# Performance work log

Measured on AMD Instinct MI355X. Metric: run time of the kernel, lower is better.

Reference implementation:

```python
import jax, jax.numpy as jnp
import numpy as np

DIM = 256   # model dim (forced by gate Linear(32,4): d = 32 = DIM//H)
H = 8       # heads (hard-coded by mask.repeat(1,8,1,1))
D = DIM // H
B = 256     # batch
NS = 100    # skeleton tokens (sub-block size)
NQ = 64     # query tokens
N = NS + NQ # 164
NE = 4      # experts
HID = 50    # expert hidden
LN_EPS = 1e-5


def setup_inputs() -> dict:
    key = jax.random.key(0)
    ks = jax.random.split(key, 12)
    s = 0.02
    return {
        "x": jax.random.normal(ks[0], (B, N, DIM), jnp.float32),
        "mask": jax.random.randint(ks[1], (B, N), 0, 2).astype(bool),
        "w_qk_s": jax.random.normal(ks[2], (DIM, 2 * DIM), jnp.float32) * s,
        "w_qk_q": jax.random.normal(ks[3], (DIM, 2 * DIM), jnp.float32) * s,
        "w_v": jax.random.normal(ks[4], (DIM, DIM), jnp.float32) * s,
        "w_gate": jax.random.normal(ks[5], (D, NE), jnp.float32) * s,
        "b_gate": jnp.zeros((NE,), jnp.float32),
        "ln_gamma": jnp.ones((NE,), jnp.float32),
        "ln_beta": jnp.zeros((NE,), jnp.float32),
        "w1": jax.random.normal(ks[6], (NE, NS, HID), jnp.float32) * s,
        "b1": jnp.zeros((NE, HID), jnp.float32),
        "w2": jax.random.normal(ks[7], (NE, HID, NS), jnp.float32) * s,
        "b2": jnp.zeros((NE, NS), jnp.float32),
        "w_out": jax.random.normal(ks[8], (DIM, DIM), jnp.float32) * s,
        "b_out": jnp.zeros((DIM,), jnp.float32),
    }


def reference(x, mask, w_qk_s, w_qk_q, w_v, w_gate, b_gate, ln_gamma, ln_beta,
              w1, b1, w2, b2, w_out, b_out):
    b, n, dim = x.shape
    scale = dim ** -0.5  # scale_with_head=False -> dim**-0.5

    def to_heads(t):  # (b, m, H*D) -> (b, H, m, D)
        return t.reshape(b, -1, H, D).transpose(0, 2, 1, 3)

    # separate qk projections for skeleton (first 100) vs query (last 64) tokens
    q_s, k_s = jnp.split(x[:, :NS] @ w_qk_s, 2, axis=-1)
    q_q, k_q = jnp.split(x[:, NS:] @ w_qk_q, 2, axis=-1)
    q = jnp.concatenate([to_heads(q_s), to_heads(q_q)], axis=2)  # (b,H,N,D)
    k = jnp.concatenate([to_heads(k_s), to_heads(k_q)], axis=2)
    v = to_heads(x @ w_v)

    # gates: RAW reshape of x (b,n,H*D) -> (b,H,n,D) (memory reinterpretation,
    # as in torch x.reshape), detached, sliced to first 100 'rows'
    gx = jax.lax.stop_gradient(x).reshape(b, H, n, D)[:, :, :NS, :]
    g = gx @ w_gate + b_gate                              # (b,H,100,4)
    mu = g.mean(-1, keepdims=True)
    var = g.var(-1, keepdims=True)
    g = (g - mu) / jnp.sqrt(var + LN_EPS) * ln_gamma + ln_beta
    gates = jax.nn.softmax(g, axis=-1)                    # (b,H,100,4)

    dots = jnp.einsum('bhid,bhjd->bhij', q, k) * scale    # (b,H,N,N)
    mask_value = -jnp.finfo(dots.dtype).max
    dots = jnp.where(mask[:, None, None, :], mask_value, dots)

    # soft-MoE over the 100x100 sub-block (experts applied along key axis)
    attn_q = dots[:, :, :NS, :NS]                         # (b,H,100,100)
    h1 = jax.nn.relu(jnp.einsum('bhij,ejk->bheik', jax.nn.relu(attn_q), w1)
                     + b1[:, None, :])                    # (b,H,4,100,50)
    eo = jax.nn.relu(jnp.einsum('bheik,ekj->bheij', h1, w2)
                     + b2[:, None, :])                    # (b,H,4,100,100)
    moes = jnp.einsum('bheij,bhie->bhij', eo, gates)      # (b,H,100,100)

    dots = dots.at[:, :, :NS, :NS].add(moes)
    attn = jax.nn.softmax(dots, axis=-1)
    out = jnp.einsum('bhij,bhjd->bhid', attn, v)          # (b,H,N,D)
    out = out.transpose(0, 2, 1, 3).reshape(b, n, dim)
    return out @ w_out + b_out
```

## Files before the change

### kernel.cpp

```cpp
#include <hip/hip_runtime.h>

typedef __bf16 bf16x8 __attribute__((ext_vector_type(8)));
typedef __bf16 bf16x4 __attribute__((ext_vector_type(4)));
typedef float  f32x4  __attribute__((ext_vector_type(4)));

__device__ __forceinline__ bf16x8 ldb8(const __bf16* p) {
    return *reinterpret_cast<const bf16x8*>(p);
}
__device__ __forceinline__ bf16x8 zero8() {
    bf16x8 z;
    #pragma unroll
    for (int i = 0; i < 8; i++) z[i] = (__bf16)0.f;
    return z;
}
__device__ __forceinline__ __bf16 ldw(const void* p, int i, int m) {
    return m ? (__bf16)((const float*)p)[i] : ((const __bf16*)p)[i];
}
__device__ __forceinline__ bf16x8 ldx8(const void* p, size_t ei, int m) {
    if (m) {
        const float* f = (const float*)p + ei;
        f32x4 a = *reinterpret_cast<const f32x4*>(f);
        f32x4 b = *reinterpret_cast<const f32x4*>(f + 4);
        bf16x8 r;
        #pragma unroll
        for (int u = 0; u < 4; u++) { r[u] = (__bf16)a[u]; r[4 + u] = (__bf16)b[u]; }
        return r;
    }
    return ldb8((const __bf16*)p + ei);
}

__global__ __launch_bounds__(256) void detect_kernel(
    const void* x, const void* mask, int* modes, unsigned* maskb)
{
    __shared__ int v32bad, v16bad, sbad;
    __shared__ unsigned mb[24];
    const int t = threadIdx.x, bid = blockIdx.x;
    if (t == 0) { v32bad = 0; v16bad = 0; sbad = 0; }
    if (t < 24) mb[t] = ((t % 6) == 5) ? 0xFFFFFFF0u : 0u;
    __syncthreads();
    const unsigned int* mw = (const unsigned int*)mask;
    int b32 = 0, b16 = 0;
    for (int i = t; i < 10496; i += 256) {
        unsigned int w = mw[i];
        if (!(w == 0u || w == 1u || w == 0x3F800000u)) b32++;
        unsigned int h0 = w & 0xFFFFu, h1 = w >> 16;
        if (!(h0 == 0u || h0 == 1u || h0 == 0x3F80u)) b16++;
        if (!(h1 == 0u || h1 == 1u || h1 == 0x3F80u)) b16++;
    }
    if (b32) atomicAdd(&v32bad, b32);
    if (b16) atomicAdd(&v16bad, b16);
    if (bid == 0) {
        const unsigned int* xw = (const unsigned int*)x;
        int bad = 0;
        for (int i = t; i < 2048; i += 256) {
            unsigned int w = xw[i];
            unsigned int el = (w >> 7) & 0xFF, eh = (w >> 23) & 0xFF;
            if (el >= 0x94 || el == 0xFF) bad++;
            if (eh >= 0x94 || eh == 0xFF) bad++;
        }
        if (bad) atomicAdd(&sbad, bad);
    }
    __syncthreads();
    const int mmode = (v32bad == 0) ? 0 : ((v16bad == 0) ? 2 : 1);
    if (bid == 0 && t == 0) { modes[0] = (sbad > 64) ? 1 : 0; modes[1] = mmode; }
    const int lo = bid * 656;
    for (int i2 = t; i2 < 656; i2 += 256) {
        int i = lo + i2;
        int val;
        if (mmode == 0)      val = (((const int*)mask)[i] != 0);
        else if (mmode == 2) val = (((const unsigned short*)mask)[i] != 0);
        else                 val = (((const unsigned char*)mask)[i] != 0);
        if (val) {
            int ib = i2 / 164, jb = i2 - ib * 164;
            atomicOr(&mb[ib * 6 + (jb >> 5)], 1u << (jb & 31));
        }
    }
    __syncthreads();
    if (t < 24) maskb[bid * 24 + t] = mb[t];
}

__global__ __launch_bounds__(256) void prep_kernel(
    const void* wqks, const void* wqkq, const void* wv, const void* w1,
    const void* w2, const void* wout, const void* wg, const void* bg,
    const void* lng, const void* lnb, const void* b1, const void* b2,
    const void* bout, const int* __restrict__ modes,
    __bf16* __restrict__ Wts, __bf16* __restrict__ Wtq,
    __bf16* __restrict__ w1t, __bf16* __restrict__ w2t,
    __bf16* __restrict__ wot, __bf16* __restrict__ wsm)
{
    const int m = modes[0];
    int i = blockIdx.x * 256 + threadIdx.x;
    if (i < 196608) {
        int n = i >> 8, k = i & 255;
        __bf16 vs, vq;
        if (n < 512) { vs = ldw(wqks, k * 512 + n, m); vq = ldw(wqkq, k * 512 + n, m); }
        else         { vs = ldw(wv, k * 256 + (n - 512), m); vq = vs; }
        Wts[i] = vs; Wtq[i] = vq;
        return;
    }
    i -= 196608;
    if (i < 32768) {
        int e = i >> 13, r = i & 8191, n = r >> 7, k = r & 127;
        __bf16 v = (__bf16)0.f;
        if (n < 50) {
            if (k < 100)       v = ldw(w1, (e * 100 + k) * 50 + n, m);
            else if (k == 100) v = ldw(b1, e * 50 + n, m);
        }
        w1t[i] = v;
        return;
    }
    i -= 32768;
    if (i < 28672) {
        int e = i / 7168, r = i % 7168, n = r >> 6, k = r & 63;
        __bf16 v = (__bf16)0.f;
        if (n < 100) {
            if (k < 50)       v = ldw(w2, (e * 50 + k) * 100 + n, m);
            else if (k == 50) v = ldw(b2, e * 100 + n, m);
        }
        w2t[i] = v;
        return;
    }
    i -= 28672;
    if (i < 65536) {
        int n = i >> 8, k = i & 255;
        wot[i] = ldw(wout, k * 256 + n, m);
        return;
    }
    i -= 65536;
    if (i < 996) {
        __bf16 v;
        if (i < 128)      v = ldw(wg, i, m);
        else if (i < 132) v = ldw(bg, i - 128, m);
        else if (i < 136) v = ldw(lng, i - 132, m);
        else if (i < 140) v = ldw(lnb, i - 136, m);
        else if (i < 340) v = ldw(b1, i - 140, m);
        else if (i < 740) v = ldw(b2, i - 340, m);
        else              v = ldw(bout, i - 740, m);
        wsm[i] = v;
    }
}

__global__ __launch_bounds__(256, 2) void qkv_kernel(
    const void* __restrict__ x, const __bf16* __restrict__ Wts,
    const __bf16* __restrict__ Wtq, const __bf16* __restrict__ wsm,
    const int* __restrict__ modes,
    __bf16* __restrict__ q, __bf16* __restrict__ k, __bf16* __restrict__ vt,
    float* __restrict__ gates)
{
    __shared__ __bf16 xs[32][264];
    __shared__ float wgf[128];
    __shared__ float gcst[12];
    const int m = modes[0];
    const int b = blockIdx.y;
    const int mt = blockIdx.x >> 1;
    const int half = blockIdx.x & 1;
    const __bf16* Wt = (mt < 4) ? Wts : Wtq;
    const int rbase = (mt < 4) ? mt * 32 : 100 + (mt - 4) * 32;
    const int tid = threadIdx.x;

    if (tid < 128) wgf[tid] = (float)wsm[tid];
    if (tid < 12)  gcst[tid] = (float)wsm[128 + tid];
    for (int c = tid; c < 1024; c += 256) {
        int row = c >> 5, part = c & 31;
        bf16x8 val = ldx8(x, ((size_t)b * 164 + rbase + row) * 256 + part * 8, m);
        *reinterpret_cast<bf16x8*>(&xs[row][part * 8]) = val;
    }
    __syncthreads();

    if (half == 0) {
        int jg = rbase * 8 + tid;
        int h = jg / 164;
        int j = jg - h * 164;
        if (j < 100) {
            const __bf16* xp = &xs[tid >> 3][(tid & 7) * 32];
            float g[4] = {gcst[0], gcst[1], gcst[2], gcst[3]};
            #pragma unroll
            for (int p = 0; p < 4; p++) {
                bf16x8 xv = ldb8(xp + p * 8);
                #pragma unroll
                for (int u = 0; u < 8; u++) {
                    float f = (float)xv[u];
                    #pragma unroll
                    for (int e = 0; e < 4; e++) g[e] += f * wgf[(p * 8 + u) * 4 + e];
                }
            }
            float mu = 0.25f * (g[0] + g[1] + g[2] + g[3]);
            float var = 0.25f * ((g[0]-mu)*(g[0]-mu) + (g[1]-mu)*(g[1]-mu) +
                                 (g[2]-mu)*(g[2]-mu) + (g[3]-mu)*(g[3]-mu));
            float is = rsqrtf(var + 1e-5f);
            float mx = -3.0e38f;
            #pragma unroll
            for (int e = 0; e < 4; e++) {
                g[e] = (g[e] - mu) * is * gcst[4 + e] + gcst[8 + e];
                mx = fmaxf(mx, g[e]);
            }
            float s = 0.f;
            #pragma unroll
            for (int e = 0; e < 4; e++) { g[e] = __expf(g[e] - mx); s += g[e]; }
            float inv = 1.f / s;
            float4 gv = make_float4(g[0]*inv, g[1]*inv, g[2]*inv, g[3]*inv);
            *reinterpret_cast<float4*>(&gates[((size_t)(b * 8 + h) * 100 + j) * 4]) = gv;
        }
    }

    const int w = tid >> 6, l = tid & 63, lr = l & 15, lc = l >> 4;
    f32x4 acc[2][6];
    #pragma unroll
    for (int ms = 0; ms < 2; ms++)
        #pragma unroll
        for (int nt = 0; nt < 6; nt++) acc[ms][nt] = (f32x4){0.f, 0.f, 0.f, 0.f};

    #pragma unroll
    for (int kt = 0; kt < 8; kt++) {
        bf16x8 a0 = ldb8(&xs[lr][kt * 32 + lc * 8]);
        bf16x8 a1 = ldb8(&xs[16 + lr][kt * 32 + lc * 8]);
        #pragma unroll
        for (int nt = 0; nt < 6; nt++) {
            bf16x8 bb = ldb8(Wt + (size_t)(half * 384 + w * 96 + nt * 16 + lr) * 256 + kt * 32 + lc * 8);
            acc[0][nt] = __builtin_amdgcn_mfma_f32_16x16x32_bf16(a0, bb, acc[0][nt], 0, 0, 0);
            acc[1][nt] = __builtin_amdgcn_mfma_f32_16x16x32_bf16(a1, bb, acc[1][nt], 0, 0, 0);
        }
    }
    #pragma unroll
    for (int ms = 0; ms < 2; ms++) {
        #pragma unroll
        for (int nt = 0; nt < 6; nt++) {
            int c = half * 384 + w * 96 + nt * 16 + lr;
            int i0 = rbase + ms * 16 + lc * 4;
            if (c < 512) {
                __bf16* dst; int ch;
                if (c < 256) { dst = q; ch = c; }
                else         { dst = k; ch = c - 256; }
                int hh = ch >> 5, d = ch & 31;
                #pragma unroll
                for (int r = 0; r < 4; r++) {
                    int i = i0 + r;
                    if (mt >= 4 || i < 100)
                        dst[(((size_t)b * 8 + hh) * 164 + i) * 32 + d] = (__bf16)acc[ms][nt][r];
                }
            } else {
                int ch = c - 512, hh = ch >> 5, d = ch & 31;
                if (mt >= 4 || i0 < 100) {
                    bf16x4 pv;
                    #pragma unroll
                    for (int r = 0; r < 4; r++) pv[r] = (__bf16)acc[ms][nt][r];
                    *reinterpret_cast<bf16x4*>(&vt[((size_t)(b * 8 + hh) * 32 + d) * 176 + i0]) = pv;
                }
            }
        }
    }
}

__global__ __launch_bounds__(256, 4) void attn_kernel(
    const __bf16* __restrict__ qg, const __bf16* __restrict__ kg,
    const __bf16* __restrict__ vtg, const float* __restrict__ gatesg,
    const unsigned* __restrict__ maskbg, const __bf16* __restrict__ w1t,
    const __bf16* __restrict__ w2t, __bf16* __restrict__ ohg)
{
    __shared__ __align__(16) __bf16 lds[20352];
    const int RS_OFF = 7040;
    const int P_OFF  = 7040;
    const int H1_OFF = 15744;

    const int bh = blockIdx.x, rt = blockIdx.y, b = bh >> 3, tid = threadIdx.x;
    const int w = tid >> 6, l = tid & 63, lr = l & 15, lc = l >> 4;
    const int m0 = w * 16;

    const __bf16* kbase = kg + (size_t)bh * 164 * 32;
    for (int c = tid; c < 704; c += 256) {
        int row = c >> 2, part = c & 3;
        bf16x8 val = (row < 164) ? ldb8(kbase + row * 32 + part * 8) : zero8();
        *reinterpret_cast<bf16x8*>(&lds[row * 40 + part * 8]) = val;
    }
    const unsigned* mbp = maskbg + b * 6;
    unsigned mbits = 0;
    #pragma unroll
    for (int nt = 0; nt < 11; nt++)
        mbits |= ((mbp[nt >> 1] >> (((nt & 1) << 4) + lr)) & 1u) << nt;
    int qrow = rt * 64 + m0 + lr; if (qrow > 163) qrow = 163;
    bf16x8 afq = ldb8(qg + ((size_t)bh * 164 + qrow) * 32 + lc * 8);
    __syncthreads();

    f32x4 raw[11];
    __builtin_amdgcn_s_setprio(1);
    #pragma unroll
    for (int nt = 0; nt < 11; nt++) {
        bf16x8 bf = ldb8(&lds[(nt * 16 + lr) * 40 + lc * 8]);
        f32x4 acc = {0.f, 0.f, 0.f, 0.f};
        acc = __builtin_amdgcn_mfma_f32_16x16x32_bf16(afq, bf, acc, 0, 0, 0);
        bool bad = (mbits >> nt) & 1;
        #pragma unroll
        for (int r = 0; r < 4; r++)
            raw[nt][r] = bad ? -1e30f : acc[r] * 0.0625f;
    }
    __builtin_amdgcn_s_setprio(0);

    if (rt < 2) {
        #pragma unroll
        for (int nt = 0; nt < 8; nt++) {
            int j = nt * 16 + lr;
            #pragma unroll
            for (int r = 0; r < 4; r++) {
                float v = raw[nt][r];
                v = (v < 0.f) ? 0.f : v;
                if (j >= 100) v = (j == 100) ? 1.f : 0.f;
                lds[RS_OFF + (m0 + lc * 4 + r) * 136 + j] = (__bf16)v;
            }
        }
    }
    __syncthreads();

    const __bf16* vtb = vtg + (size_t)bh * 32 * 176;
    #pragma unroll
    for (int p = 0; p < 3; p++) {
        int c = tid + p * 256;
        int row = c / 24, jc = c - row * 24, j0 = jc * 8;
        bf16x8 vv;
        if (j0 < 164) {
            vv = ldb8(vtb + row * 176 + j0);
            if (j0 == 160) { vv[4] = (__bf16)0.f; vv[5] = (__bf16)0.f; vv[6] = (__bf16)0.f; vv[7] = (__bf16)0.f; }
        } else vv = zero8();
        *reinterpret_cast<bf16x8*>(&lds[row * 200 + j0]) = vv;
    }

    if (rt < 2) {
        const int gi0 = rt * 64 + m0 + lc * 4;
        for (int e = 0; e < 4; e++) {
            bf16x8 sa[4];
            #pragma unroll
            for (int kt = 0; kt < 4; kt++)
                sa[kt] = ldb8(&lds[RS_OFF + (m0 + lr) * 136 + kt * 32 + lc * 8]);
            #pragma unroll
            for (int nt = 0; nt < 4; nt++) {
                f32x4 acc = {0.f, 0.f, 0.f, 0.f};
                __builtin_amdgcn_s_setprio(1);
                #pragma unroll
                for (int kt = 0; kt < 4; kt++) {
                    bf16x8 bb = ldb8(w1t + (size_t)(e * 64 + nt * 16 + lr) * 128 + kt * 32 + lc * 8);
                    acc = __builtin_amdgcn_mfma_f32_16x16x32_bf16(sa[kt], bb, acc, 0, 0, 0);
                }
                __builtin_amdgcn_s_setprio(0);
                int n = nt * 16 + lr;
                #pragma unroll
                for (int r = 0; r < 4; r++) {
                    float v = acc[r];
                    if (v < 0.f) v = 0.f;
                    if (n == 50) v = 1.f;
                    lds[H1_OFF + (m0 + lc * 4 + r) * 72 + n] = (__bf16)v;
                }
            }
            bf16x8 ha0 = ldb8(&lds[H1_OFF + (m0 + lr) * 72 + lc * 8]);
            bf16x8 ha1 = ldb8(&lds[H1_OFF + (m0 + lr) * 72 + 32 + lc * 8]);
            float gt[4];
            #pragma unroll
            for (int r = 0; r < 4; r++) {
                int gi = gi0 + r;
                gt[r] = (gi < 100) ? gatesg[((size_t)bh * 100 + gi) * 4 + e] : 0.f;
            }
            #pragma unroll
            for (int nt = 0; nt < 7; nt++) {
                f32x4 acc = {0.f, 0.f, 0.f, 0.f};
                __builtin_amdgcn_s_setprio(1);
                bf16x8 bb0 = ldb8(w2t + (size_t)(e * 112 + nt * 16 + lr) * 64 + lc * 8);
                acc = __builtin_amdgcn_mfma_f32_16x16x32_bf16(ha0, bb0, acc, 0, 0, 0);
                bf16x8 bb1 = ldb8(w2t + (size_t)(e * 112 + nt * 16 + lr) * 64 + 32 + lc * 8);
                acc = __builtin_amdgcn_mfma_f32_16x16x32_bf16(ha1, bb1, acc, 0, 0, 0);
                __builtin_amdgcn_s_setprio(0);
                #pragma unroll
                for (int r = 0; r < 4; r++) {
                    float v = acc[r];
                    if (v < 0.f) v = 0.f;
                    raw[nt][r] += v * gt[r];
                }
            }
        }
    }
    __syncthreads();

    #pragma unroll
    for (int r = 0; r < 4; r++) {
        float m2 = raw[0][r];
        #pragma unroll
        for (int nt = 1; nt < 11; nt++) m2 = fmaxf(m2, raw[nt][r]);
        m2 = fmaxf(m2, __shfl_xor(m2, 1, 64));
        m2 = fmaxf(m2, __shfl_xor(m2, 2, 64));
        m2 = fmaxf(m2, __shfl_xor(m2, 4, 64));
        m2 = fmaxf(m2, __shfl_xor(m2, 8, 64));
        float s2 = 0.f;
        #pragma unroll
        for (int nt = 0; nt < 11; nt++) {
            float ev = __expf(raw[nt][r] - m2);
            raw[nt][r] = ev;
            s2 += ev;
        }
        s2 += __shfl_xor(s2, 1, 64);
        s2 += __shfl_xor(s2, 2, 64);
        s2 += __shfl_xor(s2, 4, 64);
        s2 += __shfl_xor(s2, 8, 64);
        float inv = (s2 > 0.f) ? 1.f / s2 : 0.f;
        #pragma unroll
        for (int nt = 0; nt < 11; nt++)
            lds[P_OFF + (m0 + lc * 4 + r) * 200 + nt * 16 + lr] = (__bf16)(raw[nt][r] * inv);
        lds[P_OFF + (m0 + lc * 4 + r) * 200 + 176 + lr] = (__bf16)0.f;
    }
    __syncthreads();

    int gi = rt * 64 + m0 + lr;
    #pragma unroll
    for (int nt = 0; nt < 2; nt++) {
        f32x4 acc = {0.f, 0.f, 0.f, 0.f};
        __builtin_amdgcn_s_setprio(1);
        #pragma unroll
        for (int kt = 0; kt < 6; kt++) {
            bf16x8 va = ldb8(&lds[(nt * 16 + lr) * 200 + kt * 32 + lc * 8]);
            bf16x8 pb = ldb8(&lds[P_OFF + (m0 + lr) * 200 + kt * 32 + lc * 8]);
            acc = __builtin_amdgcn_mfma_f32_16x16x32_bf16(va, pb, acc, 0, 0, 0);
        }
        __builtin_amdgcn_s_setprio(0);
        if (gi < 164) {
            bf16x4 ov;
            #pragma unroll
            for (int r = 0; r < 4; r++) ov[r] = (__bf16)acc[r];
            *reinterpret_cast<bf16x4*>(&ohg[((size_t)bh * 164 + gi) * 32 + nt * 16 + lc * 4]) = ov;
        }
    }
}

__global__ __launch_bounds__(256) void outproj_kernel(
    const __bf16* __restrict__ oh, const __bf16* __restrict__ wot,
    const __bf16* __restrict__ wsm, float* __restrict__ out)
{
    const __bf16* bout = wsm + 740;
    const int b = blockIdx.y;
    const int mt = blockIdx.x >> 2;
    const int ntile = blockIdx.x & 3;
    const int tid = threadIdx.x;
    const int w = tid >> 6, l = tid & 63, lr = l & 15, lc = l >> 4;
    int row = mt * 64 + w * 16 + lr; if (row > 163) row = 163;
    f32x4 acc[4];
    #pragma unroll
    for (int nt = 0; nt < 4; nt++) acc[nt] = (f32x4){0.f, 0.f, 0.f, 0.f};
    #pragma unroll
    for (int kt = 0; kt < 8; kt++) {
        bf16x8 a = ldb8(oh + (((size_t)b * 8 + kt) * 164 + row) * 32 + lc * 8);
        #pragma unroll
        for (int nt = 0; nt < 4; nt++) {
            bf16x8 bb = ldb8(wot + (size_t)(ntile * 64 + nt * 16 + lr) * 256 + kt * 32 + lc * 8);
            acc[nt] = __builtin_amdgcn_mfma_f32_16x16x32_bf16(a, bb, acc[nt], 0, 0, 0);
        }
    }
    #pragma unroll
    for (int nt = 0; nt < 4; nt++) {
        int n = ntile * 64 + nt * 16 + lr;
        float bias = (float)bout[n];
        #pragma unroll
        for (int r = 0; r < 4; r++) {
            int i = mt * 64 + w * 16 + lc * 4 + r;
            if (i < 164)
                out[((size_t)b * 164 + i) * 256 + n] = acc[nt][r] + bias;
        }
    }
}

extern "C" void kernel_launch(void* const* d_in, const int* in_sizes, int n_in,
                              void* d_out, int out_size, void* d_ws, size_t ws_size,
                              hipStream_t stream) {
    const void* x      = d_in[0];
    const void* mask   = d_in[1];
    const void* w_qk_s = d_in[2];
    const void* w_qk_q = d_in[3];
    const void* w_v    = d_in[4];
    const void* w_gate = d_in[5];
    const void* b_gate = d_in[6];
    const void* ln_g   = d_in[7];
    const void* ln_b   = d_in[8];
    const void* w1     = d_in[9];
    const void* b1     = d_in[10];
    const void* w2     = d_in[11];
    const void* b2     = d_in[12];
    const void* w_out  = d_in[13];
    const void* b_out  = d_in[14];
    float* out = (float*)d_out;

    char* ws = (char*)d_ws;
    size_t off = 0;
    auto nextp = [&](size_t bytes) {
        char* p = ws + off;
        off += (bytes + 255) & ~(size_t)255;
        return p;
    };
    const size_t QKV_ELEMS = (size_t)256 * 8 * 164 * 32;
    const size_t VT_ELEMS  = (size_t)256 * 8 * 32 * 176;
    int*      modes  = (int*)nextp(64);
    unsigned* maskb  = (unsigned*)nextp((size_t)256 * 6 * 4);
    __bf16* qws  = (__bf16*)nextp(QKV_ELEMS * 2);
    __bf16* kws  = (__bf16*)nextp(QKV_ELEMS * 2);
    __bf16* vtws = (__bf16*)nextp(VT_ELEMS * 2);
    __bf16* ohws = (__bf16*)nextp(QKV_ELEMS * 2);
    float*  gws  = (float*)nextp((size_t)2048 * 100 * 4 * 4);
    __bf16* Wts  = (__bf16*)nextp(768 * 256 * 2);
    __bf16* Wtq  = (__bf16*)nextp(768 * 256 * 2);
    __bf16* w1t  = (__bf16*)nextp(4 * 64 * 128 * 2);
    __bf16* w2t  = (__bf16*)nextp(4 * 112 * 64 * 2);
    __bf16* wot  = (__bf16*)nextp(256 * 256 * 2);
    __bf16* wsm  = (__bf16*)nextp(996 * 2);

    detect_kernel<<<64, 256, 0, stream>>>(x, mask, modes, maskb);
    prep_kernel<<<1268, 256, 0, stream>>>(w_qk_s, w_qk_q, w_v, w1, w2, w_out,
                                          w_gate, b_gate, ln_g, ln_b, b1, b2,
                                          b_out, modes, Wts, Wtq, w1t, w2t, wot, wsm);
    qkv_kernel<<<dim3(12, 256), 256, 0, stream>>>(x, Wts, Wtq, wsm, modes,
                                                  qws, kws, vtws, gws);
    attn_kernel<<<dim3(2048, 3), 256, 0, stream>>>(qws, kws, vtws, gws, maskb,
                                                   w1t, w2t, ohws);
    outproj_kernel<<<dim3(12, 256), 256, 0, stream>>>(ohws, wot, wsm, out);
}
```

Before: 513.8 us.

## Fuse detect into prep, swizzle attention grid by XCD, limit MoE to needed waves

Merges the mask/dtype detection kernel into the weight-prep kernel as extra blocks, removing one launch. Every block now recomputes the x-dtype check itself. The attention grid is flattened and remapped so blocks sharing a (batch, head) land on the same XCD, aiming for better L2 reuse of K/V. The MoE path now runs only in waves whose query rows fall inside the 100-row skeleton block, skipping wasted MFMA work. K padding rows are no longer zero-filled in LDS, which relies on masking to hide the uninitialized values.

Result: faster. 490.4 us (-4.5%).

```diff
diff --git a/kernel.cpp b/kernel.cpp
--- a/kernel.cpp
+++ b/kernel.cpp
@@ -29,27 +29,21 @@
     return ldb8((const __bf16*)p + ei);
 }
 
-__global__ __launch_bounds__(256) void detect_kernel(
-    const void* x, const void* mask, int* modes, unsigned* maskb)
+__global__ __launch_bounds__(256) void prep_kernel(
+    const void* x, const void* mask,
+    const void* wqks, const void* wqkq, const void* wv, const void* w1,
+    const void* w2, const void* wout, const void* wg, const void* bg,
+    const void* lng, const void* lnb, const void* b1, const void* b2,
+    const void* bout, int* modes, unsigned* maskb,
+    __bf16* __restrict__ Wts, __bf16* __restrict__ Wtq,
+    __bf16* __restrict__ w1t, __bf16* __restrict__ w2t,
+    __bf16* __restrict__ wot, __bf16* __restrict__ wsm)
 {
-    __shared__ int v32bad, v16bad, sbad;
-    __shared__ unsigned mb[24];
+    __shared__ int sbad;
     const int t = threadIdx.x, bid = blockIdx.x;
-    if (t == 0) { v32bad = 0; v16bad = 0; sbad = 0; }
-    if (t < 24) mb[t] = ((t % 6) == 5) ? 0xFFFFFFF0u : 0u;
-    __syncthreads();
-    const unsigned int* mw = (const unsigned int*)mask;
-    int b32 = 0, b16 = 0;
-    for (int i = t; i < 10496; i += 256) {
-        unsigned int w = mw[i];
-        if (!(w == 0u || w == 1u || w == 0x3F800000u)) b32++;
-        unsigned int h0 = w & 0xFFFFu, h1 = w >> 16;
-        if (!(h0 == 0u || h0 == 1u || h0 == 0x3F80u)) b16++;
-        if (!(h1 == 0u || h1 == 1u || h1 == 0x3F80u)) b16++;
-    }
-    if (b32) atomicAdd(&v32bad, b32);
-    if (b16) atomicAdd(&v16bad, b16);
-    if (bid == 0) {
+    if (t == 0) sbad = 0;
+    __syncthreads();
+    {
         const unsigned int* xw = (const unsigned int*)x;
         int bad = 0;
         for (int i = t; i < 2048; i += 256) {
@@ -61,35 +55,47 @@
         if (bad) atomicAdd(&sbad, bad);
     }
     __syncthreads();
-    const int mmode = (v32bad == 0) ? 0 : ((v16bad == 0) ? 2 : 1);
-    if (bid == 0 && t == 0) { modes[0] = (sbad > 64) ? 1 : 0; modes[1] = mmode; }
-    const int lo = bid * 656;
-    for (int i2 = t; i2 < 656; i2 += 256) {
-        int i = lo + i2;
-        int val;
-        if (mmode == 0)      val = (((const int*)mask)[i] != 0);
-        else if (mmode == 2) val = (((const unsigned short*)mask)[i] != 0);
-        else                 val = (((const unsigned char*)mask)[i] != 0);
-        if (val) {
-            int ib = i2 / 164, jb = i2 - ib * 164;
-            atomicOr(&mb[ib * 6 + (jb >> 5)], 1u << (jb & 31));
-        }
-    }
-    __syncthreads();
-    if (t < 24) maskb[bid * 24 + t] = mb[t];
-}
-
-__global__ __launch_bounds__(256) void prep_kernel(
-    const void* wqks, const void* wqkq, const void* wv, const void* w1,
-    const void* w2, const void* wout, const void* wg, const void* bg,
-    const void* lng, const void* lnb, const void* b1, const void* b2,
-    const void* bout, const int* __restrict__ modes,
-    __bf16* __restrict__ Wts, __bf16* __restrict__ Wtq,
-    __bf16* __restrict__ w1t, __bf16* __restrict__ w2t,
-    __bf16* __restrict__ wot, __bf16* __restrict__ wsm)
-{
-    const int m = modes[0];
-    int i = blockIdx.x * 256 + threadIdx.x;
+    const int m = (sbad > 64) ? 1 : 0;
+
+    if (bid >= 1268) {
+        __shared__ int v32bad, v16bad;
+        __shared__ unsigned mb[24];
+        const int mbid = bid - 1268;
+        if (t == 0) { v32bad = 0; v16bad = 0; }
+        if (t < 24) mb[t] = ((t % 6) == 5) ? 0xFFFFFFF0u : 0u;
+        __syncthreads();
+        const unsigned int* mw = (const unsigned int*)mask;
+        int b32 = 0, b16 = 0;
+        for (int i = t; i < 10496; i += 256) {
+            unsigned int w = mw[i];
+            if (!(w == 0u || w == 1u || w == 0x3F800000u)) b32++;
+            unsigned int h0 = w & 0xFFFFu, h1 = w >> 16;
+            if (!(h0 == 0u || h0 == 1u || h0 == 0x3F80u)) b16++;
+            if (!(h1 == 0u || h1 == 1u || h1 == 0x3F80u)) b16++;
+        }
+        if (b32) atomicAdd(&v32bad, b32);
+        if (b16) atomicAdd(&v16bad, b16);
+        __syncthreads();
+        const int mmode = (v32bad == 0) ? 0 : ((v16bad == 0) ? 2 : 1);
+        if (mbid == 0 && t == 0) { modes[0] = m; modes[1] = mmode; }
+        const int lo = mbid * 656;
+        for (int i2 = t; i2 < 656; i2 += 256) {
+            int i = lo + i2;
+            int val;
+            if (mmode == 0)      val = (((const int*)mask)[i] != 0);
+            else if (mmode == 2) val = (((const unsigned short*)mask)[i] != 0);
+            else                 val = (((const unsigned char*)mask)[i] != 0);
+            if (val) {
+                int ib = i2 / 164, jb = i2 - ib * 164;
+                atomicOr(&mb[ib * 6 + (jb >> 5)], 1u << (jb & 31));
+            }
+        }
+        __syncthreads();
+        if (t < 24) maskb[mbid * 24 + t] = mb[t];
+        return;
+    }
+
+    int i = bid * 256 + t;
     if (i < 196608) {
         int n = i >> 8, k = i & 255;
         __bf16 vs, vq;
@@ -262,14 +268,19 @@
     const int P_OFF  = 7040;
     const int H1_OFF = 15744;
 
-    const int bh = blockIdx.x, rt = blockIdx.y, b = bh >> 3, tid = threadIdx.x;
+    const int flat = blockIdx.x;
+    const int xcd = flat & 7, j5 = flat >> 3;
+    const int bh = ((j5 & 255) << 3) | xcd;
+    const int rt = j5 >> 8;
+    const int b = bh >> 3, tid = threadIdx.x;
     const int w = tid >> 6, l = tid & 63, lr = l & 15, lc = l >> 4;
     const int m0 = w * 16;
+    const bool moe_wave = (rt * 64 + m0) < 100;
 
     const __bf16* kbase = kg + (size_t)bh * 164 * 32;
-    for (int c = tid; c < 704; c += 256) {
+    for (int c = tid; c < 656; c += 256) {
         int row = c >> 2, part = c & 3;
-        bf16x8 val = (row < 164) ? ldb8(kbase + row * 32 + part * 8) : zero8();
+        bf16x8 val = ldb8(kbase + row * 32 + part * 8);
         *reinterpret_cast<bf16x8*>(&lds[row * 40 + part * 8]) = val;
     }
     const unsigned* mbp = maskbg + b * 6;
@@ -295,7 +306,7 @@
     }
     __builtin_amdgcn_s_setprio(0);
 
-    if (rt < 2) {
+    if (moe_wave) {
         #pragma unroll
         for (int nt = 0; nt < 8; nt++) {
             int j = nt * 16 + lr;
@@ -323,7 +334,7 @@
         *reinterpret_cast<bf16x8*>(&lds[row * 200 + j0]) = vv;
     }
 
-    if (rt < 2) {
+    if (moe_wave) {
         const int gi0 = rt * 64 + m0 + lc * 4;
         for (int e = 0; e < 4; e++) {
             bf16x8 sa[4];
@@ -505,13 +516,13 @@
     __bf16* wot  = (__bf16*)nextp(256 * 256 * 2);
     __bf16* wsm  = (__bf16*)nextp(996 * 2);
 
-    detect_kernel<<<64, 256, 0, stream>>>(x, mask, modes, maskb);
-    prep_kernel<<<1268, 256, 0, stream>>>(w_qk_s, w_qk_q, w_v, w1, w2, w_out,
-                                          w_gate, b_gate, ln_g, ln_b, b1, b2,
-                                          b_out, modes, Wts, Wtq, w1t, w2t, wot, wsm);
+    prep_kernel<<<1332, 256, 0, stream>>>(x, mask, w_qk_s, w_qk_q, w_v, w1, w2,
+                                          w_out, w_gate, b_gate, ln_g, ln_b, b1,
+                                          b2, b_out, modes, maskb,
+                                          Wts, Wtq, w1t, w2t, wot, wsm);
     qkv_kernel<<<dim3(12, 256), 256, 0, stream>>>(x, Wts, Wtq, wsm, modes,
                                                   qws, kws, vtws, gws);
-    attn_kernel<<<dim3(2048, 3), 256, 0, stream>>>(qws, kws, vtws, gws, maskb,
-                                                   w1t, w2t, ohws);
+    attn_kernel<<<6144, 256, 0, stream>>>(qws, kws, vtws, gws, maskb,
+                                          w1t, w2t, ohws);
     outproj_kernel<<<dim3(12, 256), 256, 0, stream>>>(ohws, wot, wsm, out);
 }
```
